# Kernel tuning notes

Measured on AMD Instinct MI355X. Metric: run time of the kernel, lower is better.

The kernel has to match this reference:

```python
import jax, jax.numpy as jnp
import numpy as np

B_, L, HID = 2, 1024, 2048
N, H, P, NA = 128, 64, 64, 32   # state, heads, head_dim, rope angle pairs
DIN = 2 * H * P + 2 * N + 3 * H + NA  # 8672
EPS = 1e-5
A_FLOOR = 1e-4


def setup_inputs() -> dict:
    key = jax.random.key(0)
    k0, k1, k2 = jax.random.split(key, 3)
    hidden_states = jax.random.normal(k0, (B_, L, HID), jnp.float32)
    in_proj_w = jax.random.normal(k1, (DIN, HID), jnp.float32) * 0.02
    out_proj_w = jax.random.normal(k2, (HID, H * P), jnp.float32) * 0.02
    # dt_bias init exactly as in the torch module
    rng = np.random.default_rng(0)
    dt = np.exp(rng.random(H) * (np.log(0.1) - np.log(0.001)) + np.log(0.001))
    dt = np.clip(dt, 1e-4, None)
    dt_bias = jnp.asarray(dt + np.log(-np.expm1(-dt)), jnp.float32)
    return {
        'hidden_states': hidden_states,
        'in_proj_w': in_proj_w,
        'dt_bias': dt_bias,
        'B_bias': jnp.ones((H, N), jnp.float32),
        'C_bias': jnp.ones((H, N), jnp.float32),
        'B_norm_w': jnp.ones((N,), jnp.float32),
        'C_norm_w': jnp.ones((N,), jnp.float32),
        'D': jnp.ones((H,), jnp.float32),
        'out_proj_w': out_proj_w,
    }


def _rmsnorm(x, w):
    var = jnp.mean(jnp.square(x), axis=-1, keepdims=True)
    return x * jax.lax.rsqrt(var + EPS) * w


def _forward(hidden_states, in_proj_w, dt_bias, B_bias, C_bias,
             B_norm_w, C_norm_w, D, out_proj_w):
    b, l, _ = hidden_states.shape
    proj = hidden_states @ in_proj_w.T  # (b,l,DIN)
    splits = np.cumsum([H * P, H * P, N, N, H, H, H])
    z, x, Braw, Craw, dd_dt, dd_A, trap, angles = jnp.split(proj, splits, axis=-1)
    z = z.reshape(b, l, H, P)
    x = x.reshape(b, l, H, P)
    # data-dependent A (per token, per head), clamped
    A = jnp.minimum(-jax.nn.softplus(dd_A.astype(jnp.float32)), -A_FLOOR)
    DT = jax.nn.softplus(dd_dt + dt_bias)          # (b,l,H)
    decay = jnp.exp(A * DT)                        # (b,l,H)
    lam = jax.nn.sigmoid(trap)                     # trapezoidal weight (b,l,H)
    # RMSNorm then per-head input-independent bias (n_groups=1, mimo_rank=1)
    Bn = _rmsnorm(Braw, B_norm_w)[:, :, None, :] + B_bias  # (b,l,H,N)
    Cn = _rmsnorm(Craw, C_norm_w)[:, :, None, :] + C_bias  # (b,l,H,N)
    # blockwise rotary on first 2*NA state dims, cumulative data-dependent phase
    phase = jnp.cumsum(angles[:, :, None, :].astype(jnp.float32) * DT[..., None], axis=1)  # (b,l,H,NA)
    cos, sin = jnp.cos(phase), jnp.sin(phase)

    def rope(v):
        v1, v2, rest = v[..., :NA], v[..., NA:2 * NA], v[..., 2 * NA:]
        return jnp.concatenate([v1 * cos - v2 * sin, v1 * sin + v2 * cos, rest], axis=-1)

    Bh = rope(Bn.astype(jnp.float32))
    Ch = rope(Cn.astype(jnp.float32))
    u = (x * DT[..., None]).astype(jnp.float32)    # (b,l,H,P)

    # selective scan with generalized trapezoidal discretization:
    # h_t = a_t h_{t-1} + (1-lam_t) u_t B_t^T + lam_t a_t u_{t-1} B_{t-1}^T
    def step(carry, inp):
        h, Gp = carry
        Bt, Ct, ut, dec, lm = inp
        G = ut[..., :, None] * Bt[..., None, :]    # (b,H,P,N)
        h = dec[..., None, None] * h + (1.0 - lm)[..., None, None] * G \
            + (lm * dec)[..., None, None] * Gp
        y = jnp.einsum('bhpn,bhn->bhp', h, Ct)
        return (h, G), y

    h0 = jnp.zeros((b, H, P, N), jnp.float32)
    xs = (Bh.transpose(1, 0, 2, 3), Ch.transpose(1, 0, 2, 3),
          u.transpose(1, 0, 2, 3), decay.transpose(1, 0, 2), lam.transpose(1, 0, 2))
    _, ys = jax.lax.scan(step, (h0, h0), xs)       # (l,b,H,P)
    y = ys.transpose(1, 0, 2, 3)
    y = y + D[None, None, :, None] * x             # skip connection
    y = y * jax.nn.silu(z)                         # output gate (Z path in kernel)
    y = y.reshape(b, l, H * P)
    return y @ out_proj_w.T


def reference(hidden_states, in_proj_w, dt_bias, B_bias, C_bias,
              B_norm_w, C_norm_w, D, out_proj_w):
    return _forward(hidden_states, in_proj_w, dt_bias, B_bias, C_bias,
                    B_norm_w, C_norm_w, D, out_proj_w)
```

## Files before the change

### kernel.cpp

```cpp
#include <hip/hip_runtime.h>
#include <hip/hip_bf16.h>
#include <cstdint>
#include <cstddef>

#define DEVINL __device__ __forceinline__

typedef __attribute__((ext_vector_type(8))) short bf16x8;
typedef __attribute__((ext_vector_type(4))) float f32x4;

DEVINL float bf2f(unsigned short u){
  union { unsigned u32; float f; } cv; cv.u32 = ((unsigned)u) << 16; return cv.f;
}
DEVINL unsigned short f2bf(float f){
  union { float f; unsigned u32; } cv; cv.f = f;
  unsigned u = cv.u32;
  return (unsigned short)((u + 0x7FFFu + ((u >> 16) & 1u)) >> 16);
}
DEVINL float softplusf(float x){ return x > 20.f ? x : log1pf(expf(x)); }

DEVINL void g2l16(const void* gptr, void* ldsptr){
  __builtin_amdgcn_global_load_lds(
      (const __attribute__((address_space(1))) unsigned int*)gptr,
      (__attribute__((address_space(3))) unsigned int*)(uintptr_t)ldsptr,
      16, 0, 0);
}

DEVINL int swzb(int row, int col){ return row*256 + ((col*2) ^ ((row&7)<<4)); }
DEVINL void ldsw_write8(unsigned short* b, int row, int col, bf16x8 v){
  *(bf16x8*)((char*)b + swzb(row,col)) = v;
}
DEVINL bf16x8 ldsw_read8(const unsigned short* b, int row, int col){
  return *(const bf16x8*)((const char*)b + swzb(row,col));
}
DEVINL void ldsw_write1(unsigned short* b, int row, int col, unsigned short v){
  *(unsigned short*)((char*)b + swzb(row,col)) = v;
}
DEVINL unsigned short ldsw_read1(const unsigned short* b, int row, int col){
  return *(const unsigned short*)((const char*)b + swzb(row,col));
}

__global__ __launch_bounds__(256) void k_f32_to_bf16(
    const float* __restrict__ in, unsigned short* __restrict__ out, long n)
{
  long i = ((long)blockIdx.x * 256 + threadIdx.x) * 4;
  if (i + 3 < n){
    float4 v = *(const float4*)(in + i);
    unsigned long long pk =
        (unsigned long long)f2bf(v.x)
      | ((unsigned long long)f2bf(v.y) << 16)
      | ((unsigned long long)f2bf(v.z) << 32)
      | ((unsigned long long)f2bf(v.w) << 48);
    *(unsigned long long*)(out + i) = pk;
  }
}

template<bool OUT_BF16>
__global__ __launch_bounds__(256) void k_gemm_bt(
    const unsigned short* __restrict__ A,
    const unsigned short* __restrict__ Bt,
    void* __restrict__ Cout,
    int K, int Nrows, int Npad, int tiles_n)
{
  __shared__ unsigned short Asub[128*32];
  __shared__ unsigned short Bsub[128*32];
  const int tid = threadIdx.x;
  const int rt = blockIdx.x / tiles_n, ct = blockIdx.x % tiles_n;
  const int lane = tid & 63, wave = tid >> 6;
  const int wr = wave >> 1, wc = wave & 1;

  const int sr = tid >> 2;
  const int sc = (tid & 3) * 8;
  const size_t a_r0 = (size_t)(rt*128 + sr) * K + sc;
  const size_t a_r1 = a_r0 + (size_t)64 * K;
  int b0 = ct*128 + sr;      if (b0 > Nrows-1) b0 = Nrows-1;
  int b1 = ct*128 + 64 + sr; if (b1 > Nrows-1) b1 = Nrows-1;
  const size_t b_r0 = (size_t)b0 * K + sc;
  const size_t b_r1 = (size_t)b1 * K + sc;

  char* aL0 = (char*)Asub + tid*16;
  char* aL1 = (char*)Asub + 4096 + tid*16;
  char* bL0 = (char*)Bsub + tid*16;
  char* bL1 = (char*)Bsub + 4096 + tid*16;

  f32x4 acc[4][4] = {};
  const int fr = lane & 15;
  const int fk = (lane >> 4) * 8;

  for (int k0 = 0; k0 < K; k0 += 32){
    g2l16(A  + a_r0 + k0, aL0);
    g2l16(A  + a_r1 + k0, aL1);
    g2l16(Bt + b_r0 + k0, bL0);
    g2l16(Bt + b_r1 + k0, bL1);
    asm volatile("s_waitcnt vmcnt(0)" ::: "memory");
    __syncthreads();

    bf16x8 af[4], bfr[4];
    #pragma unroll
    for (int i = 0; i < 4; i++){
      af[i]  = *(const bf16x8*)&Asub[(wr*64 + i*16 + fr)*32 + fk];
      bfr[i] = *(const bf16x8*)&Bsub[(wc*64 + i*16 + fr)*32 + fk];
    }
    #pragma unroll
    for (int mi = 0; mi < 4; mi++)
      #pragma unroll
      for (int ni = 0; ni < 4; ni++)
        acc[mi][ni] = __builtin_amdgcn_mfma_f32_16x16x32_bf16(af[mi], bfr[ni], acc[mi][ni], 0, 0, 0);
    __syncthreads();
  }

  const int er = (lane >> 4) * 4;
  const int ec = lane & 15;
  #pragma unroll
  for (int mi = 0; mi < 4; mi++){
    #pragma unroll
    for (int ni = 0; ni < 4; ni++){
      const int row = rt*128 + wr*64 + mi*16 + er;
      const int col = ct*128 + wc*64 + ni*16 + ec;
      #pragma unroll
      for (int r = 0; r < 4; r++){
        if (OUT_BF16)
          ((unsigned short*)Cout)[(size_t)(row+r)*Npad + col] = f2bf(acc[mi][ni][r]);
        else
          ((float*)Cout)[(size_t)(row+r)*Npad + col] = acc[mi][ni][r];
      }
    }
  }
}

__global__ __launch_bounds__(256) void k_prep_scalars(
    const unsigned short* __restrict__ proj, const float* __restrict__ dt_bias,
    float* __restrict__ DTt, float* __restrict__ logdec, float* __restrict__ lamt)
{
  int idx = blockIdx.x*256 + threadIdx.x;
  int h = idx & 63, row = idx >> 6;
  int b = row >> 10, l = row & 1023;
  size_t base = (size_t)row * 8704;
  float dd_dt = bf2f(proj[base + 8448 + h]);
  float dd_A  = bf2f(proj[base + 8512 + h]);
  float trap  = bf2f(proj[base + 8576 + h]);
  float DT = softplusf(dd_dt + dt_bias[h]);
  float A  = -fmaxf(softplusf(dd_A), 1e-4f);
  size_t o = ((size_t)(b*64 + h))*1024 + l;
  DTt[o]    = DT;
  logdec[o] = A * DT;
  lamt[o]   = 1.f / (1.f + expf(-trap));
}

__global__ __launch_bounds__(128) void k_rmsnorm(
    const unsigned short* __restrict__ proj, const float* __restrict__ Bw,
    const float* __restrict__ Cw, unsigned short* __restrict__ Bb2,
    unsigned short* __restrict__ Cb2)
{
  int row = blockIdx.x, n = threadIdx.x;
  size_t base = (size_t)row * 8704;
  float bv = bf2f(proj[base + 8192 + n]);
  float cv = bf2f(proj[base + 8320 + n]);
  float sb = bv*bv, sc = cv*cv;
  #pragma unroll
  for (int m = 1; m < 64; m <<= 1){ sb += __shfl_xor(sb, m, 64); sc += __shfl_xor(sc, m, 64); }
  __shared__ float red[4];
  if ((n & 63) == 0){ red[(n>>6)*2] = sb; red[(n>>6)*2+1] = sc; }
  __syncthreads();
  sb = red[0] + red[2];
  sc = red[1] + red[3];
  float rb = rsqrtf(sb*(1.f/128.f) + 1e-5f);
  float rc = rsqrtf(sc*(1.f/128.f) + 1e-5f);
  Bb2[row*128 + n] = f2bf(bv*rb*Bw[n]);
  Cb2[row*128 + n] = f2bf(cv*rc*Cw[n]);
}

__global__ __launch_bounds__(256) void k_chunkscan(
    const float* __restrict__ logdec, const float* __restrict__ lamt,
    float* __restrict__ clcb, float* __restrict__ gb)
{
  int bh = blockIdx.x;
  size_t base = (size_t)bh * 1024;
  int tid = threadIdx.x;
  int e0 = tid * 4;
  float v0 = logdec[base+e0], v1 = logdec[base+e0+1], v2 = logdec[base+e0+2], v3 = logdec[base+e0+3];
  float p0 = v0, p1 = p0+v1, p2 = p1+v2, p3 = p2+v3;
  float tot = p3;
  int sub = tid & 31;
  float incl = tot;
  #pragma unroll
  for (int off = 1; off < 32; off <<= 1){
    float u = __shfl_up(incl, off, 32);
    if (sub >= off) incl += u;
  }
  float excl = incl - tot;
  clcb[base+e0]   = excl + p0;
  clcb[base+e0+1] = excl + p1;
  clcb[base+e0+2] = excl + p2;
  clcb[base+e0+3] = excl + p3;
  #pragma unroll
  for (int i = 0; i < 4; i++){
    int l = e0 + i;
    int ln = (l == 1023) ? 1023 : l + 1;
    gb[base+l] = 1.f - lamt[base+l] + lamt[base+ln];
  }
}

__global__ __launch_bounds__(256) void k_phase(
    const unsigned short* __restrict__ proj, const float* __restrict__ DTt,
    unsigned short* __restrict__ cosb, unsigned short* __restrict__ sinb)
{
  int bh = blockIdx.x, b = bh >> 6, h = bh & 63;
  int na = threadIdx.x & 31, c = threadIdx.x >> 5;
  __shared__ float part[8][32];
  const float* dtr = DTt + (size_t)bh * 1024;
  float s = 0.f;
  for (int i = 0; i < 128; i++){
    int l = c*128 + i; int row = b*1024 + l;
    float ang = bf2f(proj[(size_t)row*8704 + 8640 + na]);
    s = fmaf(ang, dtr[l], s);
  }
  part[c][na] = s;
  __syncthreads();
  float off = 0.f;
  for (int cc = 0; cc < c; cc++) off += part[cc][na];
  float ph = off;
  for (int i = 0; i < 128; i++){
    int l = c*128 + i; int row = b*1024 + l;
    float ang = bf2f(proj[(size_t)row*8704 + 8640 + na]);
    ph = fmaf(ang, dtr[l], ph);
    float sn, cs;
    __sincosf(ph, &sn, &cs);
    size_t o = ((size_t)row*64 + h)*32 + na;
    cosb[o] = f2bf(cs); sinb[o] = f2bf(sn);
  }
}

__global__ __launch_bounds__(256, 1) void k_intra(
    const unsigned short* __restrict__ proj,
    const unsigned short* __restrict__ Bb2, const unsigned short* __restrict__ Cb2,
    const float* __restrict__ Bbias, const float* __restrict__ Cbias,
    const unsigned short* __restrict__ cosb, const unsigned short* __restrict__ sinb,
    const float* __restrict__ DTt, const float* __restrict__ clcb,
    const float* __restrict__ gb, const float* __restrict__ lamt,
    const float* __restrict__ Dv, unsigned short* __restrict__ ybf,
    unsigned short* __restrict__ Gbuf)
{
  const int c = blockIdx.x & 7, bh = blockIdx.x >> 3;
  const int b = bh >> 6, h = bh & 63;
  const int tid = threadIdx.x, lane = tid & 63, wave = tid >> 6;
  const int wr = wave >> 1, wc = wave & 1;
  const int fr = lane & 15, fq = lane >> 4;

  __shared__ __align__(16) unsigned short Cs[128*128];
  __shared__ __align__(16) unsigned short Bs[128*128];
  __shared__ __align__(16) unsigned short BTs[128*128];
  __shared__ __align__(16) unsigned short Uts[64*128];
  __shared__ float clcs[128], lams[128], gs[128], wUs[128], dts[128];
  __shared__ float biasB[128], biasC[128];

  const int base = b*1024 + c*128;
  const size_t shbase = (size_t)bh * 1024;
  const float Dh = Dv[h];

  if (tid < 128){
    int l = c*128 + tid;
    clcs[tid] = clcb[shbase + l];
    dts[tid]  = DTt[shbase + l];
    lams[tid] = lamt[shbase + l];
    gs[tid]   = gb[shbase + l];
    biasB[tid] = Bbias[h*128 + tid];
  } else {
    biasC[tid-128] = Cbias[h*128 + tid-128];
  }
  __syncthreads();
  if (tid < 128) wUs[tid] = __expf(clcs[127] - clcs[tid]) * gs[tid];

  {
    const int t = tid >> 1, half = tid & 1;
    const int grow = base + t;
    const size_t roff = (size_t)grow*128 + half*64;
    if (half == 0){
      bf16x8 cc[4], sv[4];
      #pragma unroll
      for (int i = 0; i < 4; i++){
        cc[i] = *(const bf16x8*)(cosb + ((size_t)grow*64 + h)*32 + i*8);
        sv[i] = *(const bf16x8*)(sinb + ((size_t)grow*64 + h)*32 + i*8);
      }
      #pragma unroll
      for (int i = 0; i < 4; i++){
        bf16x8 vlo = *(const bf16x8*)(Cb2 + roff + i*8);
        bf16x8 vhi = *(const bf16x8*)(Cb2 + roff + 32 + i*8);
        bf16x8 olo, ohi;
        #pragma unroll
        for (int e = 0; e < 8; e++){
          float a = bf2f((unsigned short)vlo[e]) + biasC[i*8+e];
          float d = bf2f((unsigned short)vhi[e]) + biasC[32+i*8+e];
          float cf = bf2f((unsigned short)cc[i][e]);
          float sf = bf2f((unsigned short)sv[i][e]);
          olo[e] = (short)f2bf(a*cf - d*sf);
          ohi[e] = (short)f2bf(a*sf + d*cf);
        }
        ldsw_write8(Cs, t, i*8, olo);
        ldsw_write8(Cs, t, 32 + i*8, ohi);
      }
      #pragma unroll
      for (int i = 0; i < 4; i++){
        bf16x8 vlo = *(const bf16x8*)(Bb2 + roff + i*8);
        bf16x8 vhi = *(const bf16x8*)(Bb2 + roff + 32 + i*8);
        bf16x8 olo, ohi;
        #pragma unroll
        for (int e = 0; e < 8; e++){
          float a = bf2f((unsigned short)vlo[e]) + biasB[i*8+e];
          float d = bf2f((unsigned short)vhi[e]) + biasB[32+i*8+e];
          float cf = bf2f((unsigned short)cc[i][e]);
          float sf = bf2f((unsigned short)sv[i][e]);
          olo[e] = (short)f2bf(a*cf - d*sf);
          ohi[e] = (short)f2bf(a*sf + d*cf);
        }
        ldsw_write8(Bs, t, i*8, olo);
        ldsw_write8(Bs, t, 32 + i*8, ohi);
        #pragma unroll
        for (int e = 0; e < 8; e++){
          ldsw_write1(BTs, i*8+e, t, (unsigned short)olo[e]);
          ldsw_write1(BTs, 32+i*8+e, t, (unsigned short)ohi[e]);
        }
      }
    } else {
      #pragma unroll
      for (int i = 0; i < 8; i++){
        bf16x8 v = *(const bf16x8*)(Cb2 + roff + i*8);
        bf16x8 o;
        #pragma unroll
        for (int e = 0; e < 8; e++) o[e] = (short)f2bf(bf2f((unsigned short)v[e]) + biasC[64+i*8+e]);
        ldsw_write8(Cs, t, 64 + i*8, o);
      }
      #pragma unroll
      for (int i = 0; i < 8; i++){
        bf16x8 v = *(const bf16x8*)(Bb2 + roff + i*8);
        bf16x8 o;
        #pragma unroll
        for (int e = 0; e < 8; e++) o[e] = (short)f2bf(bf2f((unsigned short)v[e]) + biasB[64+i*8+e]);
        ldsw_write8(Bs, t, 64 + i*8, o);
        #pragma unroll
        for (int e = 0; e < 8; e++) ldsw_write1(BTs, 64+i*8+e, t, (unsigned short)o[e]);
      }
    }
  }
  {
    const int p = tid & 63, jg = tid >> 6;
    #pragma unroll 4
    for (int i = 0; i < 32; i++){
      int j = jg*32 + i;
      size_t pb = (size_t)(base + j) * 8704;
      float x  = bf2f(proj[pb + 4096 + h*64 + p]);
      ldsw_write1(Uts, p, j, f2bf(x * dts[j]));
    }
  }
  __syncthreads();

  f32x4 acc1[4][4];
  #pragma unroll
  for (int mi = 0; mi < 4; mi++)
    #pragma unroll
    for (int ni = 0; ni < 4; ni++)
      acc1[mi][ni] = (f32x4){0.f,0.f,0.f,0.f};
  #pragma unroll
  for (int ks = 0; ks < 4; ks++){
    bf16x8 af[4], bj[4];
    #pragma unroll
    for (int mi = 0; mi < 4; mi++) af[mi] = ldsw_read8(Cs, wr*64+mi*16+fr, ks*32+fq*8);
    #pragma unroll
    for (int ni = 0; ni < 4; ni++) bj[ni] = ldsw_read8(Bs, wc*64+ni*16+fr, ks*32+fq*8);
    #pragma unroll
    for (int mi = 0; mi < 4; mi++)
      #pragma unroll
      for (int ni = 0; ni < 4; ni++)
        acc1[mi][ni] = __builtin_amdgcn_mfma_f32_16x16x32_bf16(af[mi], bj[ni], acc1[mi][ni], 0,0,0);
  }
  unsigned short pr[4][4][4];
  int jj[4]; float clcj[4], gj[4];
  #pragma unroll
  for (int ni = 0; ni < 4; ni++){ jj[ni] = wc*64+ni*16+fr; clcj[ni] = clcs[jj[ni]]; gj[ni] = gs[jj[ni]]; }
  #pragma unroll
  for (int mi = 0; mi < 4; mi++){
    #pragma unroll
    for (int r = 0; r < 4; r++){
      int t = wr*64+mi*16+fq*4+r;
      float ct = clcs[t], lt = lams[t];
      #pragma unroll
      for (int ni = 0; ni < 4; ni++){
        int j = jj[ni];
        float w = (j < t) ? __expf(ct - clcj[ni])*gj[ni] : ((j == t) ? (1.f - lt) : 0.f);
        pr[mi][ni][r] = f2bf(acc1[mi][ni][r] * w);
      }
    }
  }
  __syncthreads();
  #pragma unroll
  for (int mi = 0; mi < 4; mi++)
    #pragma unroll
    for (int ni = 0; ni < 4; ni++)
      #pragma unroll
      for (int r = 0; r < 4; r++)
        ldsw_write1(Bs, wr*64+mi*16+fq*4+r, wc*64+ni*16+fr, pr[mi][ni][r]);
  __syncthreads();

  f32x4 acc2[4][2];
  #pragma unroll
  for (int mi = 0; mi < 4; mi++)
    #pragma unroll
    for (int ni = 0; ni < 2; ni++)
      acc2[mi][ni] = (f32x4){0.f,0.f,0.f,0.f};
  #pragma unroll
  for (int ks = 0; ks < 4; ks++){
    bf16x8 af[4], uj[2];
    #pragma unroll
    for (int mi = 0; mi < 4; mi++) af[mi] = ldsw_read8(Bs, wr*64+mi*16+fr, ks*32+fq*8);
    #pragma unroll
    for (int ni = 0; ni < 2; ni++) uj[ni] = ldsw_read8(Uts, wc*32+ni*16+fr, ks*32+fq*8);
    #pragma unroll
    for (int mi = 0; mi < 4; mi++)
      #pragma unroll
      for (int ni = 0; ni < 2; ni++)
        acc2[mi][ni] = __builtin_amdgcn_mfma_f32_16x16x32_bf16(af[mi], uj[ni], acc2[mi][ni], 0,0,0);
  }
  f32x4 accS[2][4];
  #pragma unroll
  for (int mi = 0; mi < 2; mi++)
    #pragma unroll
    for (int ni = 0; ni < 4; ni++)
      accS[mi][ni] = (f32x4){0.f,0.f,0.f,0.f};
  #pragma unroll
  for (int ks = 0; ks < 4; ks++){
    bf16x8 au[2], bn[4];
    #pragma unroll
    for (int mi = 0; mi < 2; mi++){
      bf16x8 raw = ldsw_read8(Uts, wr*32+mi*16+fr, ks*32+fq*8);
      #pragma unroll
      for (int e = 0; e < 8; e++){
        float f = bf2f((unsigned short)raw[e]) * wUs[ks*32+fq*8+e];
        au[mi][e] = (short)f2bf(f);
      }
    }
    #pragma unroll
    for (int ni = 0; ni < 4; ni++) bn[ni] = ldsw_read8(BTs, wc*64+ni*16+fr, ks*32+fq*8);
    #pragma unroll
    for (int mi = 0; mi < 2; mi++)
      #pragma unroll
      for (int ni = 0; ni < 4; ni++)
        accS[mi][ni] = __builtin_amdgcn_mfma_f32_16x16x32_bf16(au[mi], bn[ni], accS[mi][ni], 0,0,0);
  }

  #pragma unroll
  for (int mi = 0; mi < 4; mi++){
    #pragma unroll
    for (int ni = 0; ni < 2; ni++){
      #pragma unroll
      for (int r = 0; r < 4; r++){
        int t = wr*64+mi*16+fq*4+r;
        int p = wc*32+ni*16+fr;
        float xv = bf2f(ldsw_read1(Uts, p, t)) / fmaxf(dts[t], 1e-30f);
        float o = acc2[mi][ni][r] + Dh*xv;
        ybf[(size_t)(base + t)*4096 + h*64 + p] = f2bf(o);
      }
    }
  }
  #pragma unroll
  for (int mi = 0; mi < 2; mi++)
    #pragma unroll
    for (int ni = 0; ni < 4; ni++)
      #pragma unroll
      for (int r = 0; r < 4; r++){
        int p = wr*32+mi*16+fq*4+r;
        int n = wc*64+ni*16+fr;
        Gbuf[(size_t)blockIdx.x*8192 + p*128 + n] = f2bf(accS[mi][ni][r]);
      }
}

__global__ __launch_bounds__(256) void k_scanstate(
    const float* __restrict__ clcb, unsigned short* __restrict__ Gbuf)
{
  const int bh = blockIdx.x, tid = threadIdx.x;
  float S[32];
  #pragma unroll
  for (int i = 0; i < 32; i++) S[i] = 0.f;
  const size_t gbase = (size_t)bh*65536 + (size_t)tid*32;
  for (int c = 0; c < 8; c++){
    float decEnd = __expf(clcb[(size_t)bh*1024 + c*128 + 127]);
    unsigned short* p = Gbuf + gbase + (size_t)c*8192;
    bf16x8 g[4], s[4];
    #pragma unroll
    for (int i = 0; i < 4; i++) g[i] = *(const bf16x8*)(p + i*8);
    #pragma unroll
    for (int i = 0; i < 4; i++)
      #pragma unroll
      for (int e = 0; e < 8; e++) s[i][e] = (short)f2bf(S[i*8+e]);
    #pragma unroll
    for (int i = 0; i < 4; i++) *(bf16x8*)(p + i*8) = s[i];
    #pragma unroll
    for (int i = 0; i < 4; i++)
      #pragma unroll
      for (int e = 0; e < 8; e++)
        S[i*8+e] = decEnd*S[i*8+e] + bf2f((unsigned short)g[i][e]);
  }
}

__global__ __launch_bounds__(256) void k_inter(
    const unsigned short* __restrict__ proj,
    const unsigned short* __restrict__ Cb2, const float* __restrict__ Cbias,
    const unsigned short* __restrict__ cosb, const unsigned short* __restrict__ sinb,
    const float* __restrict__ clcb, const unsigned short* __restrict__ Sprev,
    unsigned short* __restrict__ ybf)
{
  const int c = blockIdx.x & 7, bh = blockIdx.x >> 3;
  const int b = bh >> 6, h = bh & 63;
  const int tid = threadIdx.x, lane = tid & 63, wave = tid >> 6;
  const int wr = wave >> 1, wc = wave & 1;
  const int fr = lane & 15, fq = lane >> 4;

  __shared__ __align__(16) unsigned short Cs[128*128];
  __shared__ __align__(16) unsigned short Ss[64*128];
  __shared__ float expclcs[128], biasC[128];

  const int base = b*1024 + c*128;

  if (tid < 128){
    expclcs[tid] = __expf(clcb[(size_t)bh*1024 + c*128 + tid]);
    biasC[tid] = Cbias[h*128 + tid];
  }
  __syncthreads();

  {
    const int t = tid >> 1, half = tid & 1;
    const int grow = base + t;
    const size_t roff = (size_t)grow*128 + half*64;
    if (half == 0){
      bf16x8 cc[4], sv[4];
      #pragma unroll
      for (int i = 0; i < 4; i++){
        cc[i] = *(const bf16x8*)(cosb + ((size_t)grow*64 + h)*32 + i*8);
        sv[i] = *(const bf16x8*)(sinb + ((size_t)grow*64 + h)*32 + i*8);
      }
      #pragma unroll
      for (int i = 0; i < 4; i++){
        bf16x8 vlo = *(const bf16x8*)(Cb2 + roff + i*8);
        bf16x8 vhi = *(const bf16x8*)(Cb2 + roff + 32 + i*8);
        bf16x8 olo, ohi;
        #pragma unroll
        for (int e = 0; e < 8; e++){
          float a = bf2f((unsigned short)vlo[e]) + biasC[i*8+e];
          float d = bf2f((unsigned short)vhi[e]) + biasC[32+i*8+e];
          float cf = bf2f((unsigned short)cc[i][e]);
          float sf = bf2f((unsigned short)sv[i][e]);
          olo[e] = (short)f2bf(a*cf - d*sf);
          ohi[e] = (short)f2bf(a*sf + d*cf);
        }
        ldsw_write8(Cs, t, i*8, olo);
        ldsw_write8(Cs, t, 32 + i*8, ohi);
      }
    } else {
      #pragma unroll
      for (int i = 0; i < 8; i++){
        bf16x8 v = *(const bf16x8*)(Cb2 + roff + i*8);
        bf16x8 o;
        #pragma unroll
        for (int e = 0; e < 8; e++) o[e] = (short)f2bf(bf2f((unsigned short)v[e]) + biasC[64+i*8+e]);
        ldsw_write8(Cs, t, 64 + i*8, o);
      }
    }
  }
  {
    const unsigned short* src = Sprev + (size_t)blockIdx.x*8192 + (size_t)tid*32;
    #pragma unroll
    for (int i = 0; i < 4; i++){
      bf16x8 v = *(const bf16x8*)(src + i*8);
      int f = tid*32 + i*8;
      ldsw_write8(Ss, f >> 7, f & 127, v);
    }
  }
  __syncthreads();

  f32x4 acc[4][2];
  #pragma unroll
  for (int mi = 0; mi < 4; mi++)
    #pragma unroll
    for (int ni = 0; ni < 2; ni++)
      acc[mi][ni] = (f32x4){0.f,0.f,0.f,0.f};
  #pragma unroll
  for (int ks = 0; ks < 4; ks++){
    bf16x8 af[4], sj[2];
    #pragma unroll
    for (int mi = 0; mi < 4; mi++) af[mi] = ldsw_read8(Cs, wr*64+mi*16+fr, ks*32+fq*8);
    #pragma unroll
    for (int ni = 0; ni < 2; ni++) sj[ni] = ldsw_read8(Ss, wc*32+ni*16+fr, ks*32+fq*8);
    #pragma unroll
    for (int mi = 0; mi < 4; mi++)
      #pragma unroll
      for (int ni = 0; ni < 2; ni++)
        acc[mi][ni] = __builtin_amdgcn_mfma_f32_16x16x32_bf16(af[mi], sj[ni], acc[mi][ni], 0,0,0);
  }

  #pragma unroll
  for (int mi = 0; mi < 4; mi++){
    #pragma unroll
    for (int ni = 0; ni < 2; ni++){
      #pragma unroll
      for (int r = 0; r < 4; r++){
        int t = wr*64+mi*16+fq*4+r;
        int p = wc*32+ni*16+fr;
        size_t yoff = (size_t)(base + t)*4096 + h*64 + p;
        float y = bf2f(ybf[yoff]) + expclcs[t]*acc[mi][ni][r];
        float zv = bf2f(proj[(size_t)(base + t)*8704 + h*64 + p]);
        float sl = zv / (1.f + __expf(-zv));
        ybf[yoff] = f2bf(y * sl);
      }
    }
  }
}

extern "C" void kernel_launch(void* const* d_in, const int* in_sizes, int n_in,
                              void* d_out, int out_size, void* d_ws, size_t ws_size,
                              hipStream_t stream)
{
  const float* hs    = (const float*)d_in[0];
  const float* w1    = (const float*)d_in[1];
  const float* dtb   = (const float*)d_in[2];
  const float* Bbias = (const float*)d_in[3];
  const float* Cbias = (const float*)d_in[4];
  const float* Bw    = (const float*)d_in[5];
  const float* Cw    = (const float*)d_in[6];
  const float* Dv    = (const float*)d_in[7];
  const float* wo    = (const float*)d_in[8];
  float* out = (float*)d_out;
  char* ws = (char*)d_ws;

  unsigned short* projbf = (unsigned short*)(ws + 0UL);
  unsigned short* W1bf   = (unsigned short*)(ws + 35651584UL);
  unsigned short* Gbuf   = W1bf;
  unsigned short* Wobf   = W1bf;
  unsigned short* ybf    = (unsigned short*)(ws + 52428800UL);
  unsigned short* hsbf   = (unsigned short*)(ws + 71172096UL);
  unsigned short* cosb   = hsbf;
  unsigned short* sinb   = (unsigned short*)(ws + 79560704UL);
  float* DTt    = (float*)(ws + 87949312UL);
  float* logdec = (float*)(ws + 88473600UL);
  float* lamt   = (float*)(ws + 88997888UL);
  float* clcb   = (float*)(ws + 89522176UL);
  float* gb     = (float*)(ws + 90046464UL);
  unsigned short* Bb2 = (unsigned short*)(ws + 90570752UL);
  unsigned short* Cb2 = (unsigned short*)(ws + 91095040UL);
  if (ws_size < 91619328UL) return;

  (void)in_sizes; (void)n_in; (void)out_size;

  k_f32_to_bf16<<<17344, 256, 0, stream>>>(w1, W1bf, 17760256L);
  k_f32_to_bf16<<<4096,  256, 0, stream>>>(hs, hsbf, 4194304L);
  k_gemm_bt<true><<<16*68, 256, 0, stream>>>(hsbf, W1bf, projbf, 2048, 8672, 8704, 68);
  k_prep_scalars<<<512, 256, 0, stream>>>(projbf, dtb, DTt, logdec, lamt);
  k_rmsnorm<<<2048, 128, 0, stream>>>(projbf, Bw, Cw, Bb2, Cb2);
  k_chunkscan<<<128, 256, 0, stream>>>(logdec, lamt, clcb, gb);
  k_phase<<<128, 256, 0, stream>>>(projbf, DTt, cosb, sinb);
  k_intra<<<1024, 256, 0, stream>>>(projbf, Bb2, Cb2, Bbias, Cbias,
                                    cosb, sinb, DTt, clcb, gb, lamt, Dv, ybf, Gbuf);
  k_scanstate<<<128, 256, 0, stream>>>(clcb, Gbuf);
  k_inter<<<1024, 256, 0, stream>>>(projbf, Cb2, Cbias, cosb, sinb, clcb, Gbuf, ybf);
  k_f32_to_bf16<<<8192, 256, 0, stream>>>(wo, Wobf, 8388608L);
  k_gemm_bt<false><<<16*16, 256, 0, stream>>>(ybf, Wobf, out, 4096, 2048, 2048, 16);
}
```

Before: 367.7 us.

## Deepen GEMM K-tile to 64 with XOR-swizzled LDS and grouped block remap

Doubles the K-step of the bf16 MFMA GEMM tile from 32 to 64, which halves the number of barrier and wait rounds per output tile. LDS rows are XOR-swizzled by row index so the fragment reads avoid bank conflicts at the wider row stride. Block indices are remapped into eight interleaved groups when the grid is a multiple of eight, aiming for better L2 locality across workgroups. LDS use doubles, which may reduce occupancy.

Result: faster. 341.3 us (-7.2%).

```diff
diff --git a/kernel.cpp b/kernel.cpp
--- a/kernel.cpp
+++ b/kernel.cpp
@@ -61,50 +61,57 @@
     void* __restrict__ Cout,
     int K, int Nrows, int Npad, int tiles_n)
 {
-  __shared__ unsigned short Asub[128*32];
-  __shared__ unsigned short Bsub[128*32];
+  __shared__ unsigned short Asub[128*64];
+  __shared__ unsigned short Bsub[128*64];
   const int tid = threadIdx.x;
-  const int rt = blockIdx.x / tiles_n, ct = blockIdx.x % tiles_n;
+  const int nwg = gridDim.x;
+  const int wg = ((nwg & 7) == 0) ? (int)((blockIdx.x & 7) * (nwg >> 3) + (blockIdx.x >> 3))
+                                  : (int)blockIdx.x;
+  const int rt = wg / tiles_n, ct = wg % tiles_n;
   const int lane = tid & 63, wave = tid >> 6;
   const int wr = wave >> 1, wc = wave & 1;
-
-  const int sr = tid >> 2;
-  const int sc = (tid & 3) * 8;
-  const size_t a_r0 = (size_t)(rt*128 + sr) * K + sc;
-  const size_t a_r1 = a_r0 + (size_t)64 * K;
-  int b0 = ct*128 + sr;      if (b0 > Nrows-1) b0 = Nrows-1;
-  int b1 = ct*128 + 64 + sr; if (b1 > Nrows-1) b1 = Nrows-1;
-  const size_t b_r0 = (size_t)b0 * K + sc;
-  const size_t b_r1 = (size_t)b1 * K + sc;
-
-  char* aL0 = (char*)Asub + tid*16;
-  char* aL1 = (char*)Asub + 4096 + tid*16;
-  char* bL0 = (char*)Bsub + tid*16;
-  char* bL1 = (char*)Bsub + 4096 + tid*16;
+  const int fr = lane & 15;
+  const int fq = lane >> 4;
+
+  const int srow0 = tid >> 3;
+  const int sgrp  = (tid & 7) ^ ((tid >> 3) & 7);
+  size_t aoff[4], boff[4];
+  #pragma unroll
+  for (int i = 0; i < 4; i++){
+    int row = i*32 + srow0;
+    aoff[i] = (size_t)(rt*128 + row) * K + sgrp*8;
+    int brow = ct*128 + row; if (brow > Nrows-1) brow = Nrows-1;
+    boff[i] = (size_t)brow * K + sgrp*8;
+  }
 
   f32x4 acc[4][4] = {};
-  const int fr = lane & 15;
-  const int fk = (lane >> 4) * 8;
-
-  for (int k0 = 0; k0 < K; k0 += 32){
-    g2l16(A  + a_r0 + k0, aL0);
-    g2l16(A  + a_r1 + k0, aL1);
-    g2l16(Bt + b_r0 + k0, bL0);
-    g2l16(Bt + b_r1 + k0, bL1);
+
+  for (int k0 = 0; k0 < K; k0 += 64){
+    #pragma unroll
+    for (int i = 0; i < 4; i++){
+      g2l16(A  + aoff[i] + k0, (char*)Asub + (i*256 + tid)*16);
+      g2l16(Bt + boff[i] + k0, (char*)Bsub + (i*256 + tid)*16);
+    }
     asm volatile("s_waitcnt vmcnt(0)" ::: "memory");
     __syncthreads();
 
-    bf16x8 af[4], bfr[4];
-    #pragma unroll
-    for (int i = 0; i < 4; i++){
-      af[i]  = *(const bf16x8*)&Asub[(wr*64 + i*16 + fr)*32 + fk];
-      bfr[i] = *(const bf16x8*)&Bsub[(wc*64 + i*16 + fr)*32 + fk];
-    }
-    #pragma unroll
-    for (int mi = 0; mi < 4; mi++)
-      #pragma unroll
-      for (int ni = 0; ni < 4; ni++)
-        acc[mi][ni] = __builtin_amdgcn_mfma_f32_16x16x32_bf16(af[mi], bfr[ni], acc[mi][ni], 0, 0, 0);
+    #pragma unroll
+    for (int kk = 0; kk < 2; kk++){
+      bf16x8 af[4], bfr[4];
+      const int slot = (kk*4 + fq) ^ (fr & 7);
+      #pragma unroll
+      for (int i = 0; i < 4; i++){
+        int ra = wr*64 + i*16 + fr;
+        int rb = wc*64 + i*16 + fr;
+        af[i]  = *(const bf16x8*)((const char*)Asub + ra*128 + slot*16);
+        bfr[i] = *(const bf16x8*)((const char*)Bsub + rb*128 + slot*16);
+      }
+      #pragma unroll
+      for (int mi = 0; mi < 4; mi++)
+        #pragma unroll
+        for (int ni = 0; ni < 4; ni++)
+          acc[mi][ni] = __builtin_amdgcn_mfma_f32_16x16x32_bf16(af[mi], bfr[ni], acc[mi][ni], 0, 0, 0);
+    }
     __syncthreads();
   }
 
```
